# Kernel optimization log

Hardware: AMD Instinct MI355X
Metric: run time of the kernel (lower is better)

The kernel has to match this reference:

```python
import jax, jax.numpy as jnp
import numpy as np

N = 50000
E = 1600000
IN_DIM = 256
HID = 128
EPS = 1e-5


def _bn(x, gamma, beta):
    # BatchNorm1d forward in training mode: biased batch stats
    mean = jnp.mean(x, axis=0)
    var = jnp.mean((x - mean) ** 2, axis=0)
    return (x - mean) * jax.lax.rsqrt(var + EPS) * gamma + beta


def _sage(x, edge_index, Wl, bl, Wr):
    # PyG SAGEConv with mean aggregation:
    #   out = lin_l(mean_{j in N(i)} x_j) + lin_r(x_i)
    src, dst = edge_index[0], edge_index[1]
    agg = jax.ops.segment_sum(x[src], dst, num_segments=N)          # [N, H]
    cnt = jax.ops.segment_sum(jnp.ones((src.shape[0],), x.dtype), dst, num_segments=N)
    mean = agg / jnp.maximum(cnt, 1.0)[:, None]
    return mean @ Wl + bl + x @ Wr


def setup_inputs() -> dict:
    key = jax.random.key(0)
    ks = jax.random.split(key, 16)
    s_in = 1.0 / np.sqrt(IN_DIM)
    s_h = 1.0 / np.sqrt(HID)
    return {
        "x": jax.random.normal(ks[0], (N, IN_DIM), jnp.float32),
        "edge_index": jax.random.randint(ks[1], (2, E), 0, N, jnp.int32),
        # input_linear: Linear(IN_DIM, HID) + BN
        "W_in": jax.random.uniform(ks[2], (IN_DIM, HID), jnp.float32, -s_in, s_in),
        "b_in": jax.random.uniform(ks[3], (HID,), jnp.float32, -s_in, s_in),
        "g1": jnp.ones((HID,), jnp.float32), "be1": jnp.zeros((HID,), jnp.float32),
        # hidden_linear: Linear(HID, HID) + BN
        "W_hid": jax.random.uniform(ks[4], (HID, HID), jnp.float32, -s_h, s_h),
        "b_hid": jax.random.uniform(ks[5], (HID,), jnp.float32, -s_h, s_h),
        "g2": jnp.ones((HID,), jnp.float32), "be2": jnp.zeros((HID,), jnp.float32),
        # graph_conv1: SAGEConv(HID, HID) + BN
        "Wl1": jax.random.uniform(ks[6], (HID, HID), jnp.float32, -s_h, s_h),
        "bl1": jax.random.uniform(ks[7], (HID,), jnp.float32, -s_h, s_h),
        "Wr1": jax.random.uniform(ks[8], (HID, HID), jnp.float32, -s_h, s_h),
        "g3": jnp.ones((HID,), jnp.float32), "be3": jnp.zeros((HID,), jnp.float32),
        # graph_conv2: SAGEConv(HID, HID) + BN
        "Wl2": jax.random.uniform(ks[9], (HID, HID), jnp.float32, -s_h, s_h),
        "bl2": jax.random.uniform(ks[10], (HID,), jnp.float32, -s_h, s_h),
        "Wr2": jax.random.uniform(ks[11], (HID, HID), jnp.float32, -s_h, s_h),
        "g4": jnp.ones((HID,), jnp.float32), "be4": jnp.zeros((HID,), jnp.float32),
    }


def reference(x, edge_index, W_in, b_in, g1, be1, W_hid, b_hid, g2, be2,
              Wl1, bl1, Wr1, g3, be3, Wl2, bl2, Wr2, g4, be4):
    feat = jax.nn.relu(_bn(x @ W_in + b_in, g1, be1))
    feat = jax.nn.relu(_bn(feat @ W_hid + b_hid, g2, be2))
    out = _bn(_sage(feat, edge_index, Wl1, bl1, Wr1), g3, be3)
    out = _bn(_sage(out, edge_index, Wl2, bl2, Wr2), g4, be4)
    return (feat, out)
```

## Files before the change

### kernel.cpp

```cpp
#include <hip/hip_runtime.h>
#include <stdint.h>

#define NN 50000
#define EE 1600000
#define IN_DIMC 256
#define HIDC 128
#define EPSC 1e-5f

#define NB 196
#define GA 512
#define CHUNK 3125
#define STILE_SHIFT 13
#define NKEY 2048

#define NSLOT 8
#define STATS_STRIDE (NSLOT * 256)

typedef unsigned short ushort_t;
typedef __attribute__((ext_vector_type(8))) short short8;
typedef __attribute__((ext_vector_type(4))) float floatx4;

static __device__ inline ushort_t f2bf(float f) {
    unsigned int u = __float_as_uint(f);
    u = u + 0x7fffu + ((u >> 16) & 1u);
    return (ushort_t)(u >> 16);
}
static __device__ inline unsigned int pack2(float a, float b) {
    return (unsigned int)f2bf(a) | ((unsigned int)f2bf(b) << 16);
}
static __device__ inline float bf2f(unsigned int bits16) {
    return __uint_as_float(bits16 << 16);
}

__global__ __launch_bounds__(256) void tcvt_all_kernel(
    const float* __restrict__ W_in, const float* __restrict__ W_hid,
    const float* __restrict__ Wl1, const float* __restrict__ Wr1,
    const float* __restrict__ Wl2, const float* __restrict__ Wr2,
    ushort_t* __restrict__ Wt_in, ushort_t* __restrict__ Wt_hid,
    ushort_t* __restrict__ Wtl1, ushort_t* __restrict__ Wtr1,
    ushort_t* __restrict__ Wtl2, ushort_t* __restrict__ Wtr2)
{
    const int idx = blockIdx.x * 256 + threadIdx.x;
    if (idx < 32768) {
        const int n = idx >> 8;
        const int k = idx & 255;
        Wt_in[idx] = f2bf(W_in[(size_t)k * 128 + n]);
    } else if (idx < 32768 + 5 * 16384) {
        const int r = idx - 32768;
        const int seg = r / 16384;
        const int j = r - seg * 16384;
        const int n = j >> 7;
        const int k = j & 127;
        const float* W; ushort_t* Wt;
        switch (seg) {
            case 0: W = W_hid; Wt = Wt_hid; break;
            case 1: W = Wl1;  Wt = Wtl1;  break;
            case 2: W = Wr1;  Wt = Wtr1;  break;
            case 3: W = Wl2;  Wt = Wtl2;  break;
            default: W = Wr2; Wt = Wtr2;  break;
        }
        Wt[j] = f2bf(W[(size_t)k * 128 + n]);
    }
}

__global__ __launch_bounds__(512) void mfma_gemm_kernel(
    const void* __restrict__ A1, const ushort_t* __restrict__ Wt1, int K1, int a1type,
    const void* __restrict__ A2, const ushort_t* __restrict__ Wt2, int K2,
    const float* __restrict__ bias, float* __restrict__ Cf, ushort_t* __restrict__ Cb,
    int M, int affineSeg, int affineRelu,
    const float* __restrict__ preStats, const float* __restrict__ preG,
    const float* __restrict__ preBe, float* __restrict__ outStats)
{
    __shared__ ushort_t Bs[128 * 136];
    __shared__ __align__(16) float aArr[128], bArr[128];
    __shared__ float red_s[4][128], red_q[4][128];

    const int t    = threadIdx.x;
    const int lane = t & 63;
    const int wave = t >> 6;
    const int mt   = wave >> 1;
    const int nh   = wave & 1;
    const int quad = lane >> 4;
    const int l15  = lane & 15;
    const int row0 = blockIdx.x * 64;
    const int rowW = row0 + mt * 16;
    const int ksq  = quad * 8;

    if (affineSeg >= 0 && t < 128) {
        float sS = 0.0f, sQ = 0.0f;
        #pragma unroll
        for (int s8 = 0; s8 < NSLOT; s8++) {
            sS += preStats[s8 * 256 + t];
            sQ += preStats[s8 * 256 + 128 + t];
        }
        const float invM = 1.0f / (float)M;
        const float mean = sS * invM;
        float var = sQ * invM - mean * mean;
        if (var < 0.0f) var = 0.0f;
        const float s = preG[t] / sqrtf(var + EPSC);
        aArr[t] = s;
        bArr[t] = preBe[t] - mean * s;
    }

    floatx4 acc[4];
    #pragma unroll
    for (int j = 0; j < 4; j++)
        acc[j] = (floatx4){0.0f, 0.0f, 0.0f, 0.0f};

    int gr = rowW + l15;
    if (gr > M - 1) gr = M - 1;

    bool firstChunk = true;

    for (int s = 0; s < 2; s++) {
        const void*     A     = s ? A2  : A1;
        const ushort_t* Wt    = s ? Wt2 : Wt1;
        const int       K     = s ? K2  : K1;
        const int       atype = s ? 1   : a1type;
        const int       doAf  = (affineSeg == s);
        if (A == nullptr) continue;

        for (int kc = 0; kc < K; kc += 128) {
            if (!firstChunk) __syncthreads();
            firstChunk = false;

            #pragma unroll
            for (int p = 0; p < 4; p++) {
                const int idx = p * 512 + t;
                const int n   = idx >> 4;
                const int c0  = (idx & 15) * 8;
                *(uint4*)(Bs + n * 136 + c0) =
                    *(const uint4*)(Wt + (size_t)n * K + kc + c0);
            }
            __syncthreads();

            short8 afrag[4];
            if (atype == 1) {
                const ushort_t* Ab = (const ushort_t*)A;
                const size_t base = (size_t)gr * K + kc + ksq;
                #pragma unroll
                for (int ks = 0; ks < 4; ks++)
                    afrag[ks] = *(const short8*)(Ab + base + ks * 32);
                if (doAf) {
                    #pragma unroll
                    for (int ks = 0; ks < 4; ks++) {
                        const int k0 = kc + ks * 32 + ksq;
                        uint4 u = __builtin_bit_cast(uint4, afrag[ks]);
                        uint4 w;
                        unsigned int* up = (unsigned int*)&u;
                        unsigned int* wp = (unsigned int*)&w;
                        #pragma unroll
                        for (int h = 0; h < 4; h++) {
                            float lo = aArr[k0 + h * 2]     * bf2f(up[h] & 0xffffu) + bArr[k0 + h * 2];
                            float hi = aArr[k0 + h * 2 + 1] * bf2f(up[h] >> 16)     + bArr[k0 + h * 2 + 1];
                            if (affineRelu) { lo = fmaxf(lo, 0.0f); hi = fmaxf(hi, 0.0f); }
                            wp[h] = pack2(lo, hi);
                        }
                        afrag[ks] = __builtin_bit_cast(short8, w);
                    }
                }
            } else {
                const float* Af = (const float*)A;
                const size_t base = (size_t)gr * K + kc + ksq;
                #pragma unroll
                for (int ks = 0; ks < 4; ks++) {
                    float4 v0 = *(const float4*)(Af + base + ks * 32);
                    float4 v1 = *(const float4*)(Af + base + ks * 32 + 4);
                    if (doAf) {
                        const int k0 = kc + ks * 32 + ksq;
                        const float4 sa0 = *(const float4*)(aArr + k0);
                        const float4 sb0 = *(const float4*)(bArr + k0);
                        const float4 sa1 = *(const float4*)(aArr + k0 + 4);
                        const float4 sb1 = *(const float4*)(bArr + k0 + 4);
                        v0.x = sa0.x * v0.x + sb0.x;
                        v0.y = sa0.y * v0.y + sb0.y;
                        v0.z = sa0.z * v0.z + sb0.z;
                        v0.w = sa0.w * v0.w + sb0.w;
                        v1.x = sa1.x * v1.x + sb1.x;
                        v1.y = sa1.y * v1.y + sb1.y;
                        v1.z = sa1.z * v1.z + sb1.z;
                        v1.w = sa1.w * v1.w + sb1.w;
                        if (affineRelu) {
                            v0.x = fmaxf(v0.x, 0.0f); v0.y = fmaxf(v0.y, 0.0f);
                            v0.z = fmaxf(v0.z, 0.0f); v0.w = fmaxf(v0.w, 0.0f);
                            v1.x = fmaxf(v1.x, 0.0f); v1.y = fmaxf(v1.y, 0.0f);
                            v1.z = fmaxf(v1.z, 0.0f); v1.w = fmaxf(v1.w, 0.0f);
                        }
                    }
                    uint4 w;
                    w.x = pack2(v0.x, v0.y);
                    w.y = pack2(v0.z, v0.w);
                    w.z = pack2(v1.x, v1.y);
                    w.w = pack2(v1.z, v1.w);
                    afrag[ks] = __builtin_bit_cast(short8, w);
                }
            }

            #pragma unroll
            for (int ks = 0; ks < 4; ks++) {
                const int ko = ks * 32 + ksq;
                short8 b[4];
                #pragma unroll
                for (int j = 0; j < 4; j++)
                    b[j] = *(const short8*)(Bs + (nh * 64 + j * 16 + l15) * 136 + ko);
                #pragma unroll
                for (int j = 0; j < 4; j++)
                    acc[j] = __builtin_amdgcn_mfma_f32_16x16x32_bf16(
                        afrag[ks], b[j], acc[j], 0, 0, 0);
            }
        }
    }

    float s_[4], q_[4];
    #pragma unroll
    for (int j = 0; j < 4; j++) { s_[j] = 0.0f; q_[j] = 0.0f; }

    #pragma unroll
    for (int j = 0; j < 4; j++) {
        const int col = nh * 64 + j * 16 + l15;
        const float bv = bias[col];
        const int rbase = rowW + quad * 4;
        #pragma unroll
        for (int reg = 0; reg < 4; reg++) {
            const float val = acc[j][reg] + bv;
            const int r_ = rbase + reg;
            if (r_ < M) {
                if (Cf) Cf[(size_t)r_ * HIDC + col] = val;
                if (Cb) Cb[(size_t)r_ * HIDC + col] = f2bf(val);
                s_[j] += val;
                q_[j] += val * val;
            }
        }
    }
    #pragma unroll
    for (int j = 0; j < 4; j++) {
        s_[j] += __shfl_xor(s_[j], 16, 64);
        s_[j] += __shfl_xor(s_[j], 32, 64);
        q_[j] += __shfl_xor(q_[j], 16, 64);
        q_[j] += __shfl_xor(q_[j], 32, 64);
    }
    if (quad == 0) {
        #pragma unroll
        for (int j = 0; j < 4; j++) {
            red_s[mt][nh * 64 + j * 16 + l15] = s_[j];
            red_q[mt][nh * 64 + j * 16 + l15] = q_[j];
        }
    }
    __syncthreads();
    if (t < 128) {
        const float S = red_s[0][t] + red_s[1][t] + red_s[2][t] + red_s[3][t];
        const float Q = red_q[0][t] + red_q[1][t] + red_q[2][t] + red_q[3][t];
        float* slot = outStats + (blockIdx.x & (NSLOT - 1)) * 256;
        atomicAdd(&slot[t], S);
        atomicAdd(&slot[128 + t], Q);
    }
}

__global__ __launch_bounds__(256) void bn_apply_kernel(
    const float* __restrict__ src, float* __restrict__ dstF,
    ushort_t* __restrict__ dstB, const float* __restrict__ stats,
    const float* __restrict__ gamma, const float* __restrict__ beta,
    int relu, int M)
{
    __shared__ float sc[128], sh[128];
    const int t = threadIdx.x;
    if (t < 128) {
        float sS = 0.0f, sQ = 0.0f;
        #pragma unroll
        for (int s8 = 0; s8 < NSLOT; s8++) {
            sS += stats[s8 * 256 + t];
            sQ += stats[s8 * 256 + 128 + t];
        }
        const float invM = 1.0f / (float)M;
        const float mean = sS * invM;
        float var = sQ * invM - mean * mean;
        if (var < 0.0f) var = 0.0f;
        const float s = gamma[t] / sqrtf(var + EPSC);
        sc[t] = s;
        sh[t] = beta[t] - mean * s;
    }
    __syncthreads();

    const int total4 = M * HIDC / 4;
    for (int i = blockIdx.x * 256 + t; i < total4; i += gridDim.x * 256) {
        float4 v = ((const float4*)src)[i];
        const int c = (i * 4) & 127;
        v.x = v.x * sc[c]     + sh[c];
        v.y = v.y * sc[c + 1] + sh[c + 1];
        v.z = v.z * sc[c + 2] + sh[c + 2];
        v.w = v.w * sc[c + 3] + sh[c + 3];
        if (relu) {
            v.x = fmaxf(v.x, 0.0f); v.y = fmaxf(v.y, 0.0f);
            v.z = fmaxf(v.z, 0.0f); v.w = fmaxf(v.w, 0.0f);
        }
        if (dstF) ((float4*)dstF)[i] = v;
        if (dstB) {
            uint2 w;
            w.x = pack2(v.x, v.y);
            w.y = pack2(v.z, v.w);
            *(uint2*)(dstB + (size_t)i * 4) = w;
        }
    }
}

__global__ __launch_bounds__(256) void bucket_hist_kernel(
    const int* __restrict__ dstArr, int* __restrict__ hist2D)
{
    __shared__ int hist[NB];
    const int t = threadIdx.x;
    for (int i = t; i < NB; i += 256) hist[i] = 0;
    __syncthreads();
    const int e0 = blockIdx.x * CHUNK;
    const int e1 = e0 + CHUNK;
    for (int e = e0 + t; e < e1; e += 256)
        atomicAdd(&hist[dstArr[e] >> 8], 1);
    __syncthreads();
    for (int i = t; i < NB; i += 256)
        hist2D[(size_t)i * GA + blockIdx.x] = hist[i];
}

__global__ __launch_bounds__(256) void bucket_scan_kernel(
    int* __restrict__ hist2D, int* __restrict__ rowTot)
{
    __shared__ int wtot[4];
    const int b = blockIdx.x;
    const int t = threadIdx.x;
    int* row = hist2D + (size_t)b * GA;
    const int v0 = row[2 * t];
    const int v1 = row[2 * t + 1];
    const int pair = v0 + v1;
    const int lane = t & 63, w = t >> 6;
    int x = pair;
    #pragma unroll
    for (int off = 1; off < 64; off <<= 1) {
        const int y = __shfl_up(x, off);
        if (lane >= off) x += y;
    }
    if (lane == 63) wtot[w] = x;
    __syncthreads();
    int woff = 0;
    #pragma unroll
    for (int j = 0; j < 4; j++) if (j < w) woff += wtot[j];
    const int excl = x + woff - pair;
    row[2 * t]     = excl;
    row[2 * t + 1] = excl + v0;
    if (t == 255) rowTot[b] = excl + pair;
}

__global__ __launch_bounds__(256) void bucket_base_kernel(
    const int* __restrict__ rowTot, int* __restrict__ bucketBase,
    int* __restrict__ rowp)
{
    __shared__ int wtot[4];
    const int t = threadIdx.x;
    const int tot = (t < NB) ? rowTot[t] : 0;
    const int lane = t & 63, w = t >> 6;
    int x = tot;
    #pragma unroll
    for (int off = 1; off < 64; off <<= 1) {
        const int y = __shfl_up(x, off);
        if (lane >= off) x += y;
    }
    if (lane == 63) wtot[w] = x;
    __syncthreads();
    int woff = 0;
    #pragma unroll
    for (int j = 0; j < 4; j++) if (j < w) woff += wtot[j];
    const int excl = x + woff - tot;
    if (t < NB) bucketBase[t] = excl;
    if (t == 0) { bucketBase[NB] = EE; rowp[NN] = EE; }
}

__global__ __launch_bounds__(256) void bucket_scatter_kernel(
    const int* __restrict__ srcArr, const int* __restrict__ dstArr,
    const int* __restrict__ hist2D, const int* __restrict__ bucketBase,
    unsigned int* __restrict__ ebuf)
{
    __shared__ int cur[NB];
    const int t = threadIdx.x;
    for (int i = t; i < NB; i += 256)
        cur[i] = bucketBase[i] + hist2D[(size_t)i * GA + blockIdx.x];
    __syncthreads();
    const int e0 = blockIdx.x * CHUNK;
    const int e1 = e0 + CHUNK;
    for (int e = e0 + t; e < e1; e += 256) {
        const int d = dstArr[e];
        const int s = srcArr[e];
        const int p = atomicAdd(&cur[d >> 8], 1);
        ebuf[p] = ((unsigned int)s << 16) | (unsigned int)d;
    }
}

__global__ __launch_bounds__(256) void fine_sort_kernel(
    const unsigned int* __restrict__ ebuf, const int* __restrict__ bucketBase,
    int* __restrict__ rowp, ushort_t* __restrict__ col)
{
    __shared__ int cnt[NKEY];
    __shared__ int wtot[4];
    const int b = blockIdx.x;
    const int t = threadIdx.x;
    const int bb0 = bucketBase[b];
    const int bb1 = bucketBase[b + 1];
    #pragma unroll
    for (int i = 0; i < 8; i++) cnt[t * 8 + i] = 0;
    __syncthreads();
    for (int e = bb0 + t; e < bb1; e += 256) {
        const unsigned int sd = ebuf[e];
        const int key = (int)((sd & 255u) << 3) | (int)(sd >> (16 + STILE_SHIFT));
        atomicAdd(&cnt[key], 1);
    }
    __syncthreads();
    int loc[8];
    int tot = 0;
    #pragma unroll
    for (int i = 0; i < 8; i++) { loc[i] = tot; tot += cnt[t * 8 + i]; }
    const int lane = t & 63, w = t >> 6;
    int x = tot;
    #pragma unroll
    for (int off = 1; off < 64; off <<= 1) {
        const int y = __shfl_up(x, off);
        if (lane >= off) x += y;
    }
    if (lane == 63) wtot[w] = x;
    __syncthreads();
    int woff = 0;
    #pragma unroll
    for (int j = 0; j < 4; j++) if (j < w) woff += wtot[j];
    const int excl = x + woff - tot;
    const int node = b * 256 + t;
    if (node < NN) rowp[node] = bb0 + excl;
    __syncthreads();
    #pragma unroll
    for (int i = 0; i < 8; i++) cnt[t * 8 + i] = excl + loc[i];
    __syncthreads();
    for (int e = bb0 + t; e < bb1; e += 256) {
        const unsigned int sd = ebuf[e];
        const int key = (int)((sd & 255u) << 3) | (int)(sd >> (16 + STILE_SHIFT));
        const int p = atomicAdd(&cnt[key], 1);
        col[bb0 + p] = (ushort_t)(sd >> 16);
    }
}

__global__ __launch_bounds__(256) void agg_kernel(
    const ushort_t* __restrict__ F, const int* __restrict__ row_ptr,
    const ushort_t* __restrict__ col, ushort_t* __restrict__ Mout,
    const float* __restrict__ preStats, const float* __restrict__ preG,
    const float* __restrict__ preBe)
{
    const int lane = threadIdx.x & 63;
    const int wave = blockIdx.x * 4 + (threadIdx.x >> 6);
    const int nwaves = gridDim.x * 4;
    const int coff = lane * 2;

    float sc0 = 1.0f, sh0 = 0.0f, sc1 = 1.0f, sh1 = 0.0f;
    const int doAf = (preStats != nullptr);
    if (doAf) {
        float s0 = 0.0f, s1 = 0.0f, q0 = 0.0f, q1 = 0.0f;
        #pragma unroll
        for (int s8 = 0; s8 < NSLOT; s8++) {
            s0 += preStats[s8 * 256 + coff];
            s1 += preStats[s8 * 256 + coff + 1];
            q0 += preStats[s8 * 256 + 128 + coff];
            q1 += preStats[s8 * 256 + 128 + coff + 1];
        }
        const float invM = 1.0f / (float)NN;
        const float m0 = s0 * invM;
        const float m1 = s1 * invM;
        float v0 = q0 * invM - m0 * m0;
        float v1 = q1 * invM - m1 * m1;
        if (v0 < 0.0f) v0 = 0.0f;
        if (v1 < 0.0f) v1 = 0.0f;
        sc0 = preG[coff] / sqrtf(v0 + EPSC);
        sc1 = preG[coff + 1] / sqrtf(v1 + EPSC);
        sh0 = preBe[coff] - m0 * sc0;
        sh1 = preBe[coff + 1] - m1 * sc1;
    }

    for (int n = wave; n < NN; n += nwaves) {
        const int b = __builtin_amdgcn_readfirstlane(row_ptr[n]);
        const int e = __builtin_amdgcn_readfirstlane(row_ptr[n + 1]);
        const int deg = e - b;
        float accx = 0.0f, accy = 0.0f;
        int j = b;
        for (; j + 8 <= e; j += 8) {
            int s0[8];
            #pragma unroll
            for (int i = 0; i < 8; i++) s0[i] = col[j + i];
            unsigned int v0[8];
            #pragma unroll
            for (int i = 0; i < 8; i++)
                v0[i] = *(const unsigned int*)(F + (size_t)s0[i] * HIDC + coff);
            #pragma unroll
            for (int i = 0; i < 8; i++) {
                accx += bf2f(v0[i] & 0xffffu);
                accy += bf2f(v0[i] >> 16);
            }
        }
        for (; j < e; j++) {
            const unsigned int v = *(const unsigned int*)(F + (size_t)col[j] * HIDC + coff);
            accx += bf2f(v & 0xffffu);
            accy += bf2f(v >> 16);
        }
        float ox, oy;
        if (deg == 0) {
            ox = 0.0f; oy = 0.0f;
        } else {
            const float inv = 1.0f / (float)deg;
            ox = accx * inv;
            oy = accy * inv;
            if (doAf) { ox = ox * sc0 + sh0; oy = oy * sc1 + sh1; }
        }
        *(unsigned int*)(Mout + (size_t)n * HIDC + coff) = pack2(ox, oy);
    }
}

extern "C" void kernel_launch(void* const* d_in, const int* in_sizes, int n_in,
                              void* d_out, int out_size, void* d_ws, size_t ws_size,
                              hipStream_t stream)
{
    const float* x     = (const float*)d_in[0];
    const int*   ei    = (const int*)  d_in[1];
    const float* W_in  = (const float*)d_in[2];
    const float* b_in  = (const float*)d_in[3];
    const float* g1    = (const float*)d_in[4];
    const float* be1   = (const float*)d_in[5];
    const float* W_hid = (const float*)d_in[6];
    const float* b_hid = (const float*)d_in[7];
    const float* g2    = (const float*)d_in[8];
    const float* be2   = (const float*)d_in[9];
    const float* Wl1   = (const float*)d_in[10];
    const float* bl1   = (const float*)d_in[11];
    const float* Wr1   = (const float*)d_in[12];
    const float* g3    = (const float*)d_in[13];
    const float* be3   = (const float*)d_in[14];
    const float* Wl2   = (const float*)d_in[15];
    const float* bl2   = (const float*)d_in[16];
    const float* Wr2   = (const float*)d_in[17];
    const float* g4    = (const float*)d_in[18];
    const float* be4   = (const float*)d_in[19];

    const int* srcArr = ei;
    const int* dstArr = ei + EE;

    char* ws = (char*)d_ws;
    float*    bufA      = (float*)ws;    ws += (size_t)NN * HIDC * sizeof(float);
    float*    bufB      = (float*)ws;    ws += (size_t)NN * HIDC * sizeof(float);
    ushort_t* featB16   = (ushort_t*)ws; ws += (size_t)NN * HIDC * sizeof(ushort_t);
    ushort_t* o3B16     = (ushort_t*)ws; ws += (size_t)NN * HIDC * sizeof(ushort_t);
    ushort_t* aggB16    = (ushort_t*)ws; ws += (size_t)NN * HIDC * sizeof(ushort_t);
    float*    stats     = (float*)ws;    ws += 4 * STATS_STRIDE * sizeof(float);
    int*      hist2D    = (int*)ws;      ws += (size_t)NB * GA * sizeof(int);
    int*      rowTot    = (int*)ws;      ws += (NB + 4) * sizeof(int);
    int*      bucketBase= (int*)ws;      ws += (NB + 4) * sizeof(int);
    int*      rowp      = (int*)ws;      ws += (size_t)(NN + 4) * sizeof(int);
    ushort_t* colIdx    = (ushort_t*)ws; ws += (size_t)EE * sizeof(ushort_t) + 64;
    unsigned int* ebuf  = (unsigned int*)ws; ws += (size_t)EE * sizeof(unsigned int);
    ushort_t* Wt_in     = (ushort_t*)ws; ws += 128 * 256 * sizeof(ushort_t);
    ushort_t* Wt_hid    = (ushort_t*)ws; ws += 128 * 128 * sizeof(ushort_t);
    ushort_t* Wtl1      = (ushort_t*)ws; ws += 128 * 128 * sizeof(ushort_t);
    ushort_t* Wtr1      = (ushort_t*)ws; ws += 128 * 128 * sizeof(ushort_t);
    ushort_t* Wtl2      = (ushort_t*)ws; ws += 128 * 128 * sizeof(ushort_t);
    ushort_t* Wtr2      = (ushort_t*)ws; ws += 128 * 128 * sizeof(ushort_t);

    float* out0 = (float*)d_out;
    float* out1 = out0 + (size_t)NN * HIDC;

    hipMemsetAsync(stats, 0, 4 * STATS_STRIDE * sizeof(float), stream);

    tcvt_all_kernel<<<448, 256, 0, stream>>>(W_in, W_hid, Wl1, Wr1, Wl2, Wr2,
                                             Wt_in, Wt_hid, Wtl1, Wtr1, Wtl2, Wtr2);

    bucket_hist_kernel<<<GA, 256, 0, stream>>>(dstArr, hist2D);
    bucket_scan_kernel<<<NB, 256, 0, stream>>>(hist2D, rowTot);
    bucket_base_kernel<<<1, 256, 0, stream>>>(rowTot, bucketBase, rowp);
    bucket_scatter_kernel<<<GA, 256, 0, stream>>>(srcArr, dstArr, hist2D,
                                                  bucketBase, ebuf);
    fine_sort_kernel<<<NB, 256, 0, stream>>>(ebuf, bucketBase, rowp, colIdx);

    const int gemmGrid = (NN + 63) / 64;

    mfma_gemm_kernel<<<gemmGrid, 512, 0, stream>>>(
        x, Wt_in, IN_DIMC, 0, nullptr, nullptr, 0,
        b_in, bufA, nullptr, NN, -1, 0, nullptr, nullptr, nullptr,
        stats + 0 * STATS_STRIDE);

    mfma_gemm_kernel<<<gemmGrid, 512, 0, stream>>>(
        bufA, Wt_hid, HIDC, 0, nullptr, nullptr, 0,
        b_hid, bufB, nullptr, NN, 0, 1, stats + 0 * STATS_STRIDE, g1, be1,
        stats + 1 * STATS_STRIDE);

    bn_apply_kernel<<<1024, 256, 0, stream>>>(bufB, out0, featB16,
                                              stats + 1 * STATS_STRIDE, g2, be2, 1, NN);

    agg_kernel<<<4096, 256, 0, stream>>>(featB16, rowp, colIdx, aggB16,
                                         nullptr, nullptr, nullptr);
    mfma_gemm_kernel<<<gemmGrid, 512, 0, stream>>>(
        aggB16, Wtl1, HIDC, 1, featB16, Wtr1, HIDC,
        bl1, nullptr, o3B16, NN, -1, 0, nullptr, nullptr, nullptr,
        stats + 2 * STATS_STRIDE);

    agg_kernel<<<4096, 256, 0, stream>>>(o3B16, rowp, colIdx, aggB16,
                                         stats + 2 * STATS_STRIDE, g3, be3);
    mfma_gemm_kernel<<<gemmGrid, 512, 0, stream>>>(
        aggB16, Wtl2, HIDC, 1, o3B16, Wtr2, HIDC,
        bl2, bufB, nullptr, NN, 1, 0, stats + 2 * STATS_STRIDE, g3, be3,
        stats + 3 * STATS_STRIDE);

    bn_apply_kernel<<<1024, 256, 0, stream>>>(bufB, out1, nullptr,
                                              stats + 3 * STATS_STRIDE, g4, be4, 0, NN);
}
```

Measured before the change: 400.9 us.

## Store bf16 features column-group-major and gather per column group in aggregation

The bf16 feature and aggregate buffers move from row-major [N][128] to four column groups of 32 ([4][N][32]). The GEMM epilogue, BN apply and the GEMM A-loads are all updated to use this layout. Each aggregation block now handles one column group, and a wave spreads four edges across 16-lane groups before reducing them with shuffles. The intent is to shrink the gather working set per pass so it stays cache-resident and to keep more loads in flight per wave. In exchange, each edge's index is read four times, once per group, and the layout is tied to K=128 for bf16 inputs.

```diff
diff --git a/kernel.cpp b/kernel.cpp
--- a/kernel.cpp
+++ b/kernel.cpp
@@ -31,6 +31,7 @@
 static __device__ inline float bf2f(unsigned int bits16) {
     return __uint_as_float(bits16 << 16);
 }
+
 
 __global__ __launch_bounds__(256) void tcvt_all_kernel(
     const float* __restrict__ W_in, const float* __restrict__ W_hid,
@@ -137,14 +138,13 @@
             short8 afrag[4];
             if (atype == 1) {
                 const ushort_t* Ab = (const ushort_t*)A;
-                const size_t base = (size_t)gr * K + kc + ksq;
                 #pragma unroll
                 for (int ks = 0; ks < 4; ks++)
-                    afrag[ks] = *(const short8*)(Ab + base + ks * 32);
+                    afrag[ks] = *(const short8*)(Ab + ((size_t)ks * NN + gr) * 32 + ksq);
                 if (doAf) {
                     #pragma unroll
                     for (int ks = 0; ks < 4; ks++) {
-                        const int k0 = kc + ks * 32 + ksq;
+                        const int k0 = ks * 32 + ksq;
                         uint4 u = __builtin_bit_cast(uint4, afrag[ks]);
                         uint4 w;
                         unsigned int* up = (unsigned int*)&u;
@@ -167,7 +167,7 @@
                     float4 v0 = *(const float4*)(Af + base + ks * 32);
                     float4 v1 = *(const float4*)(Af + base + ks * 32 + 4);
                     if (doAf) {
-                        const int k0 = kc + ks * 32 + ksq;
+                        const int k0 = ks * 32 + ksq;
                         const float4 sa0 = *(const float4*)(aArr + k0);
                         const float4 sb0 = *(const float4*)(bArr + k0);
                         const float4 sa1 = *(const float4*)(aArr + k0 + 4);
@@ -220,13 +220,15 @@
         const int col = nh * 64 + j * 16 + l15;
         const float bv = bias[col];
         const int rbase = rowW + quad * 4;
+        const int g  = nh * 2 + (j >> 1);
+        const int cw = (j & 1) * 16 + l15;
         #pragma unroll
         for (int reg = 0; reg < 4; reg++) {
             const float val = acc[j][reg] + bv;
             const int r_ = rbase + reg;
             if (r_ < M) {
                 if (Cf) Cf[(size_t)r_ * HIDC + col] = val;
-                if (Cb) Cb[(size_t)r_ * HIDC + col] = f2bf(val);
+                if (Cb) Cb[((size_t)g * NN + r_) * 32 + cw] = f2bf(val);
                 s_[j] += val;
                 q_[j] += val * val;
             }
@@ -298,7 +300,10 @@
             uint2 w;
             w.x = pack2(v.x, v.y);
             w.y = pack2(v.z, v.w);
-            *(uint2*)(dstB + (size_t)i * 4) = w;
+            const int row = i >> 5;
+            const int g   = c >> 5;
+            const int cw  = c & 31;
+            *(uint2*)(dstB + ((size_t)g * NN + row) * 32 + cw) = w;
         }
     }
 }
@@ -443,74 +448,127 @@
 
 __global__ __launch_bounds__(256) void agg_kernel(
     const ushort_t* __restrict__ F, const int* __restrict__ row_ptr,
+    const ushort_t* __restrict__ col, ushort_t* __restrict__ Mout)
+{
+    const int lane = threadIdx.x & 63;
+    const int cg   = blockIdx.x & 3;
+    const int wv   = (blockIdx.x >> 2) * 4 + (threadIdx.x >> 6);
+    const int nw   = (gridDim.x >> 2) * 4;
+    const int es   = lane >> 4;
+    const int cp   = lane & 15;
+    const ushort_t* Fg = F + (size_t)cg * NN * 32;
+    ushort_t* Mg = Mout + (size_t)cg * NN * 32;
+
+    for (int n = wv; n < NN; n += nw) {
+        const int b = __builtin_amdgcn_readfirstlane(row_ptr[n]);
+        const int e = __builtin_amdgcn_readfirstlane(row_ptr[n + 1]);
+        const int deg = e - b;
+        float ax = 0.0f, ay = 0.0f;
+        int j = b;
+        for (; j + 8 <= e; j += 8) {
+            const int i0 = col[j + es];
+            const int i1 = col[j + 4 + es];
+            const unsigned int v0 = *(const unsigned int*)(Fg + (size_t)i0 * 32 + cp * 2);
+            const unsigned int v1 = *(const unsigned int*)(Fg + (size_t)i1 * 32 + cp * 2);
+            ax += bf2f(v0 & 0xffffu) + bf2f(v1 & 0xffffu);
+            ay += bf2f(v0 >> 16) + bf2f(v1 >> 16);
+        }
+        for (; j < e; j += 4) {
+            const int idx = j + es;
+            const int cidx = idx < e ? idx : (e - 1);
+            const int ii = col[cidx];
+            const unsigned int v = *(const unsigned int*)(Fg + (size_t)ii * 32 + cp * 2);
+            if (idx < e) {
+                ax += bf2f(v & 0xffffu);
+                ay += bf2f(v >> 16);
+            }
+        }
+        ax += __shfl_xor(ax, 16, 64);
+        ax += __shfl_xor(ax, 32, 64);
+        ay += __shfl_xor(ay, 16, 64);
+        ay += __shfl_xor(ay, 32, 64);
+        if (lane < 16) {
+            const float inv = 1.0f / (float)(deg > 1 ? deg : 1);
+            *(unsigned int*)(Mg + (size_t)n * 32 + cp * 2) = pack2(ax * inv, ay * inv);
+        }
+    }
+}
+
+__global__ __launch_bounds__(256) void agg_bn_kernel(
+    const ushort_t* __restrict__ F, const int* __restrict__ row_ptr,
     const ushort_t* __restrict__ col, ushort_t* __restrict__ Mout,
     const float* __restrict__ preStats, const float* __restrict__ preG,
     const float* __restrict__ preBe)
 {
     const int lane = threadIdx.x & 63;
-    const int wave = blockIdx.x * 4 + (threadIdx.x >> 6);
-    const int nwaves = gridDim.x * 4;
-    const int coff = lane * 2;
-
-    float sc0 = 1.0f, sh0 = 0.0f, sc1 = 1.0f, sh1 = 0.0f;
-    const int doAf = (preStats != nullptr);
-    if (doAf) {
-        float s0 = 0.0f, s1 = 0.0f, q0 = 0.0f, q1 = 0.0f;
-        #pragma unroll
-        for (int s8 = 0; s8 < NSLOT; s8++) {
-            s0 += preStats[s8 * 256 + coff];
-            s1 += preStats[s8 * 256 + coff + 1];
-            q0 += preStats[s8 * 256 + 128 + coff];
-            q1 += preStats[s8 * 256 + 128 + coff + 1];
-        }
-        const float invM = 1.0f / (float)NN;
-        const float m0 = s0 * invM;
-        const float m1 = s1 * invM;
-        float v0 = q0 * invM - m0 * m0;
-        float v1 = q1 * invM - m1 * m1;
-        if (v0 < 0.0f) v0 = 0.0f;
-        if (v1 < 0.0f) v1 = 0.0f;
-        sc0 = preG[coff] / sqrtf(v0 + EPSC);
-        sc1 = preG[coff + 1] / sqrtf(v1 + EPSC);
-        sh0 = preBe[coff] - m0 * sc0;
-        sh1 = preBe[coff + 1] - m1 * sc1;
-    }
-
-    for (int n = wave; n < NN; n += nwaves) {
+    const int cg   = blockIdx.x & 3;
+    const int wv   = (blockIdx.x >> 2) * 4 + (threadIdx.x >> 6);
+    const int nw   = (gridDim.x >> 2) * 4;
+    const int es   = lane >> 4;
+    const int cp   = lane & 15;
+    const ushort_t* Fg = F + (size_t)cg * NN * 32;
+    ushort_t* Mg = Mout + (size_t)cg * NN * 32;
+
+    const int c0 = cg * 32 + cp * 2;
+    float s0 = 0.0f, s1 = 0.0f, q0 = 0.0f, q1 = 0.0f;
+    #pragma unroll
+    for (int s8 = 0; s8 < NSLOT; s8++) {
+        s0 += preStats[s8 * 256 + c0];
+        s1 += preStats[s8 * 256 + c0 + 1];
+        q0 += preStats[s8 * 256 + 128 + c0];
+        q1 += preStats[s8 * 256 + 128 + c0 + 1];
+    }
+    const float invM = 1.0f / (float)NN;
+    const float m0 = s0 * invM;
+    const float m1 = s1 * invM;
+    float v0_ = q0 * invM - m0 * m0;
+    float v1_ = q1 * invM - m1 * m1;
+    if (v0_ < 0.0f) v0_ = 0.0f;
+    if (v1_ < 0.0f) v1_ = 0.0f;
+    const float sc0 = preG[c0] / sqrtf(v0_ + EPSC);
+    const float sc1 = preG[c0 + 1] / sqrtf(v1_ + EPSC);
+    const float sh0 = preBe[c0] - m0 * sc0;
+    const float sh1 = preBe[c0 + 1] - m1 * sc1;
+
+    for (int n = wv; n < NN; n += nw) {
         const int b = __builtin_amdgcn_readfirstlane(row_ptr[n]);
         const int e = __builtin_amdgcn_readfirstlane(row_ptr[n + 1]);
         const int deg = e - b;
-        float accx = 0.0f, accy = 0.0f;
+        float ax = 0.0f, ay = 0.0f;
         int j = b;
         for (; j + 8 <= e; j += 8) {
-            int s0[8];
-            #pragma unroll
-            for (int i = 0; i < 8; i++) s0[i] = col[j + i];
-            unsigned int v0[8];
-            #pragma unroll
-            for (int i = 0; i < 8; i++)
-                v0[i] = *(const unsigned int*)(F + (size_t)s0[i] * HIDC + coff);
-            #pragma unroll
-            for (int i = 0; i < 8; i++) {
-                accx += bf2f(v0[i] & 0xffffu);
-                accy += bf2f(v0[i] >> 16);
+            const int i0 = col[j + es];
+            const int i1 = col[j + 4 + es];
+            const unsigned int v0 = *(const unsigned int*)(Fg + (size_t)i0 * 32 + cp * 2);
+            const unsigned int v1 = *(const unsigned int*)(Fg + (size_t)i1 * 32 + cp * 2);
+            ax += bf2f(v0 & 0xffffu) + bf2f(v1 & 0xffffu);
+            ay += bf2f(v0 >> 16) + bf2f(v1 >> 16);
+        }
+        for (; j < e; j += 4) {
+            const int idx = j + es;
+            const int cidx = idx < e ? idx : (e - 1);
+            const int ii = col[cidx];
+            const unsigned int v = *(const unsigned int*)(Fg + (size_t)ii * 32 + cp * 2);
+            if (idx < e) {
+                ax += bf2f(v & 0xffffu);
+                ay += bf2f(v >> 16);
             }
         }
-        for (; j < e; j++) {
-            const unsigned int v = *(const unsigned int*)(F + (size_t)col[j] * HIDC + coff);
-            accx += bf2f(v & 0xffffu);
-            accy += bf2f(v >> 16);
-        }
-        float ox, oy;
-        if (deg == 0) {
-            ox = 0.0f; oy = 0.0f;
-        } else {
-            const float inv = 1.0f / (float)deg;
-            ox = accx * inv;
-            oy = accy * inv;
-            if (doAf) { ox = ox * sc0 + sh0; oy = oy * sc1 + sh1; }
-        }
-        *(unsigned int*)(Mout + (size_t)n * HIDC + coff) = pack2(ox, oy);
+        ax += __shfl_xor(ax, 16, 64);
+        ax += __shfl_xor(ax, 32, 64);
+        ay += __shfl_xor(ay, 16, 64);
+        ay += __shfl_xor(ay, 32, 64);
+        if (lane < 16) {
+            float ox, oy;
+            if (deg == 0) {
+                ox = 0.0f; oy = 0.0f;
+            } else {
+                const float inv = 1.0f / (float)deg;
+                ox = ax * inv * sc0 + sh0;
+                oy = ay * inv * sc1 + sh1;
+            }
+            *(unsigned int*)(Mg + (size_t)n * 32 + cp * 2) = pack2(ox, oy);
+        }
     }
 }
 
@@ -592,15 +650,14 @@
     bn_apply_kernel<<<1024, 256, 0, stream>>>(bufB, out0, featB16,
                                               stats + 1 * STATS_STRIDE, g2, be2, 1, NN);
 
-    agg_kernel<<<4096, 256, 0, stream>>>(featB16, rowp, colIdx, aggB16,
-                                         nullptr, nullptr, nullptr);
+    agg_kernel<<<4096, 256, 0, stream>>>(featB16, rowp, colIdx, aggB16);
     mfma_gemm_kernel<<<gemmGrid, 512, 0, stream>>>(
         aggB16, Wtl1, HIDC, 1, featB16, Wtr1, HIDC,
         bl1, nullptr, o3B16, NN, -1, 0, nullptr, nullptr, nullptr,
         stats + 2 * STATS_STRIDE);
 
-    agg_kernel<<<4096, 256, 0, stream>>>(o3B16, rowp, colIdx, aggB16,
-                                         stats + 2 * STATS_STRIDE, g3, be3);
+    agg_bn_kernel<<<4096, 256, 0, stream>>>(o3B16, rowp, colIdx, aggB16,
+                                            stats + 2 * STATS_STRIDE, g3, be3);
     mfma_gemm_kernel<<<gemmGrid, 512, 0, stream>>>(
         aggB16, Wtl2, HIDC, 1, o3B16, Wtr2, HIDC,
         bl2, bufB, nullptr, NN, 1, 0, stats + 2 * STATS_STRIDE, g3, be3,
```

After: 442.5 us. +10.4%, slower.
